# Performance work log

Hardware: AMD Instinct MI355X
Metric: run time of the kernel (lower is better)

Reference implementation:

```python
import jax, jax.numpy as jnp
import numpy as np

HID = 512; POOL = 4096; N_OBJ_CLS = 151; N_REL_CLS = 51; EMB = 200
N_OBJ = 1024; N_REL = 128

def conv(x, w, b, pad):
    y = jax.lax.conv_general_dilated(x, w, (1, 1), [(pad, pad), (pad, pad)],
                                     dimension_numbers=('NCHW', 'OIHW', 'NCHW'))
    return y + b[None, :, None, None]

def pool2(x):
    n, c, h, w = x.shape
    return x.reshape(n, c, h // 2, 2, w // 2, 2).mean(axis=(3, 5))

def setup_inputs() -> dict:
    ks = jax.random.split(jax.random.key(0), 40)
    s = 0.02
    d = {
        'obj_feats': jax.random.normal(ks[0], (N_OBJ, HID), jnp.float32),
        'obj_preds': jax.random.randint(ks[1], (N_OBJ,), 0, N_OBJ_CLS, jnp.int32),
        'pair_idx': jax.random.randint(ks[2], (N_REL, 2), 0, N_OBJ, jnp.int32),
        'union_features': jax.random.normal(ks[3], (N_REL, POOL), jnp.float32),
        'W_post_emb': jax.random.normal(ks[4], (HID, 2 * HID)) * s,
        'b_post_emb': jnp.zeros((2 * HID,)),
        'W_post_cat': jax.random.normal(ks[5], (2 * HID, POOL)) * s,
        'b_post_cat': jnp.zeros((POOL,)),
        'W_edge': jax.random.normal(ks[6], (POOL, HID)) * s,
        'b_edge': jnp.zeros((HID,)),
        'W_lin_rel': jax.random.normal(ks[7], (3 * HID, HID)) * s,
        'b_lin_rel': jnp.zeros((HID,)),
        'W_rel': jax.random.normal(ks[8], (HID, N_REL_CLS)) * s,
        'b_rel': jnp.zeros((N_REL_CLS,)),
        'freq_table': jax.random.normal(ks[9], (N_OBJ_CLS * N_OBJ_CLS, N_REL_CLS)) * s,
        'embed_vecs': jax.random.normal(ks[10], (N_OBJ + 1, EMB)) * 0.1,
        'cw1': jax.random.normal(ks[11], (64, 1, 5, 5)) * s, 'cb1': jnp.zeros((64,)),
        'cw2': jax.random.normal(ks[12], (128, 64, 3, 3)) * s, 'cb2': jnp.zeros((128,)),
        'cw3': jax.random.normal(ks[13], (256, 128, 3, 3)) * s, 'cb3': jnp.zeros((256,)),
        'cw4': jax.random.normal(ks[14], (512, 256, 3, 3)) * s, 'cb4': jnp.zeros((512,)),
        'cw5': jax.random.normal(ks[15], (384, 512, 1, 1)) * s, 'cb5': jnp.zeros((384,)),
        'cw6': jax.random.normal(ks[16], (4096, 384, 1, 1)) * s, 'cb6': jnp.zeros((4096,)),
        'Ww1': jax.random.normal(ks[17], (8192, 512)) * s, 'bw1': jnp.zeros((512,)),
        'Ww2': jax.random.normal(ks[18], (512, 4096)) * s, 'bw2': jnp.zeros((4096,)),
    }
    return d

def reference(obj_feats, obj_preds, pair_idx, union_features,
              W_post_emb, b_post_emb, W_post_cat, b_post_cat, W_edge, b_edge,
              W_lin_rel, b_lin_rel, W_rel, b_rel, freq_table, embed_vecs,
              cw1, cb1, cw2, cb2, cw3, cb3, cw4, cb4, cw5, cb5, cw6, cb6,
              Ww1, bw1, Ww2, bw2):
    p0 = pair_idx[:, 0]; p1 = pair_idx[:, 1]
    # post_emb -> head/tail reps, gather per pair (edge construction)
    edge_rep = obj_feats @ W_post_emb + b_post_emb          # [N_obj, 2H]
    head_rep = edge_rep[:, :HID]; tail_rep = edge_rep[:, HID:]
    prod_rep = jnp.concatenate([head_rep[p0], tail_rep[p1]], axis=-1)  # [R, 2H]
    # vision path with ctx gate
    ctx_gate = prod_rep @ W_post_cat + b_post_cat            # [R, POOL]
    visual_rep = ctx_gate * union_features
    # edge context (stand-in linear+relu projection to hidden)
    edge_feats = jax.nn.relu(visual_rep @ W_edge + b_edge)   # [R, H]
    # cat_pair fusion
    rel_sub = prod_rep[:, :HID]; rel_obj = prod_rep[:, HID:]
    rel_feats = jnp.concatenate([rel_sub, edge_feats, rel_obj], axis=-1) @ W_lin_rel + b_lin_rel
    rel_dists = rel_feats @ W_rel + b_rel                    # [R, 51]
    # frequency bias on predicted pair classes
    c0 = obj_preds[p0]; c1 = obj_preds[p1]
    rel_dists = rel_dists + freq_table[c0 * N_OBJ_CLS + c1]
    # word-image branch: outer product of pair word vectors -> conv tower (detached)
    oe = embed_vecs[p0 + 1]; se = embed_vecs[p1 + 1]         # [R, 200]
    x = (oe[:, :, None] * se[:, None, :])[:, None]           # [R, 1, 200, 200]
    x = pool2(jax.nn.relu(conv(x, cw1, cb1, 2)))             # [R, 64, 100, 100]
    x = pool2(jax.nn.relu(conv(x, cw2, cb2, 1)))             # [R, 128, 50, 50]
    x = pool2(jax.nn.relu(conv(x, cw3, cb3, 1)))             # [R, 256, 25, 25]
    x = jax.nn.relu(conv(x, cw4, cb4, 1))                    # [R, 512, 25, 25]
    x = x.mean(axis=(2, 3), keepdims=True)                   # adaptive avgpool -> [R,512,1,1]
    x = jax.nn.relu(conv(x, cw5, cb5, 0))
    x = conv(x, cw6, cb6, 0).reshape(-1, 4096)
    pwe = jax.lax.stop_gradient(x)                           # .detach() in original
    # word_feature MLP (eval: dropout off)
    h = jax.nn.relu(jnp.concatenate([pwe, union_features], axis=1) @ Ww1 + bw1)
    union_out = jax.nn.relu(h @ Ww2 + bw2)                   # [R, 4096]
    return rel_dists, union_out
```

## Files before the change

kernel.cpp:

```cpp
#include <hip/hip_runtime.h>
#include <hip/hip_bf16.h>


typedef __attribute__((ext_vector_type(8))) short  s16x8;
typedef __attribute__((ext_vector_type(4))) short  s16x4;
typedef __attribute__((ext_vector_type(4))) float  f32x4;

__device__ inline unsigned short f2bf(float f) {
    unsigned u = __builtin_bit_cast(unsigned, f);
    u = (u + 0x7FFF + ((u >> 16) & 1)) >> 16;
    return (unsigned short)u;
}
__device__ inline float bf2f(unsigned short s) {
    unsigned u = ((unsigned)s) << 16;
    return __builtin_bit_cast(float, u);
}

template<bool BT, bool RELU, bool MUL>
__global__ __launch_bounds__(256) void gemm_kernel(
    const float* __restrict__ A, const float* __restrict__ B,
    const float* __restrict__ bias, const float* __restrict__ mulp,
    float* __restrict__ C, int M, int N, int K)
{
    __shared__ float As[16][68];
    __shared__ float Bs[16][68];
    const int m0 = blockIdx.x * 64, n0 = blockIdx.y * 64;
    const int tid = threadIdx.x;
    const int ty = tid >> 4, tx = tid & 15;
    float acc[4][4] = {};
    for (int k0 = 0; k0 < K; k0 += 16) {
        {
            const int m = tid >> 2, kq = (tid & 3) << 2;
            const float4 a = *reinterpret_cast<const float4*>(A + (size_t)(m0 + m) * K + k0 + kq);
            As[kq + 0][m] = a.x; As[kq + 1][m] = a.y; As[kq + 2][m] = a.z; As[kq + 3][m] = a.w;
        }
        if (!BT) {
            const int kk = tid >> 4, nq = (tid & 15) << 2;
            const float4 b = *reinterpret_cast<const float4*>(B + (size_t)(k0 + kk) * N + n0 + nq);
            *reinterpret_cast<float4*>(&Bs[kk][nq]) = b;
        } else {
            const int nn = tid >> 2, kq = (tid & 3) << 2;
            const float4 b = *reinterpret_cast<const float4*>(B + (size_t)(n0 + nn) * K + k0 + kq);
            Bs[kq + 0][nn] = b.x; Bs[kq + 1][nn] = b.y; Bs[kq + 2][nn] = b.z; Bs[kq + 3][nn] = b.w;
        }
        __syncthreads();
#pragma unroll
        for (int k = 0; k < 16; ++k) {
            const float4 av = *reinterpret_cast<const float4*>(&As[k][ty << 2]);
            const float4 bv = *reinterpret_cast<const float4*>(&Bs[k][tx << 2]);
            acc[0][0] += av.x * bv.x; acc[0][1] += av.x * bv.y; acc[0][2] += av.x * bv.z; acc[0][3] += av.x * bv.w;
            acc[1][0] += av.y * bv.x; acc[1][1] += av.y * bv.y; acc[1][2] += av.y * bv.z; acc[1][3] += av.y * bv.w;
            acc[2][0] += av.z * bv.x; acc[2][1] += av.z * bv.y; acc[2][2] += av.z * bv.z; acc[2][3] += av.z * bv.w;
            acc[3][0] += av.w * bv.x; acc[3][1] += av.w * bv.y; acc[3][2] += av.w * bv.z; acc[3][3] += av.w * bv.w;
        }
        __syncthreads();
    }
#pragma unroll
    for (int i = 0; i < 4; ++i) {
        const int m = m0 + (ty << 2) + i;
#pragma unroll
        for (int j = 0; j < 4; ++j) {
            const int n = n0 + (tx << 2) + j;
            float v = acc[i][j] + bias[n];
            if (MUL) v *= mulp[(size_t)m * N + n];
            if (RELU) v = fmaxf(v, 0.f);
            C[(size_t)m * N + n] = v;
        }
    }
}

template<bool BT>
__global__ __launch_bounds__(256) void gemmsk_kernel(
    const float* __restrict__ A, const float* __restrict__ B,
    float* __restrict__ part, int M, int N, int K, int kchunk)
{
    __shared__ float As[16][68];
    __shared__ float Bs[16][68];
    const int m0 = blockIdx.x * 64, n0 = blockIdx.y * 64;
    const int kbeg = blockIdx.z * kchunk, kend = kbeg + kchunk;
    const int tid = threadIdx.x;
    const int ty = tid >> 4, tx = tid & 15;
    float acc[4][4] = {};
    for (int k0 = kbeg; k0 < kend; k0 += 16) {
        {
            const int m = tid >> 2, kq = (tid & 3) << 2;
            const float4 a = *reinterpret_cast<const float4*>(A + (size_t)(m0 + m) * K + k0 + kq);
            As[kq + 0][m] = a.x; As[kq + 1][m] = a.y; As[kq + 2][m] = a.z; As[kq + 3][m] = a.w;
        }
        if (!BT) {
            const int kk = tid >> 4, nq = (tid & 15) << 2;
            const float4 b = *reinterpret_cast<const float4*>(B + (size_t)(k0 + kk) * N + n0 + nq);
            *reinterpret_cast<float4*>(&Bs[kk][nq]) = b;
        } else {
            const int nn = tid >> 2, kq = (tid & 3) << 2;
            const float4 b = *reinterpret_cast<const float4*>(B + (size_t)(n0 + nn) * K + k0 + kq);
            Bs[kq + 0][nn] = b.x; Bs[kq + 1][nn] = b.y; Bs[kq + 2][nn] = b.z; Bs[kq + 3][nn] = b.w;
        }
        __syncthreads();
#pragma unroll
        for (int k = 0; k < 16; ++k) {
            const float4 av = *reinterpret_cast<const float4*>(&As[k][ty << 2]);
            const float4 bv = *reinterpret_cast<const float4*>(&Bs[k][tx << 2]);
            acc[0][0] += av.x * bv.x; acc[0][1] += av.x * bv.y; acc[0][2] += av.x * bv.z; acc[0][3] += av.x * bv.w;
            acc[1][0] += av.y * bv.x; acc[1][1] += av.y * bv.y; acc[1][2] += av.y * bv.z; acc[1][3] += av.y * bv.w;
            acc[2][0] += av.z * bv.x; acc[2][1] += av.z * bv.y; acc[2][2] += av.z * bv.z; acc[2][3] += av.z * bv.w;
            acc[3][0] += av.w * bv.x; acc[3][1] += av.w * bv.y; acc[3][2] += av.w * bv.z; acc[3][3] += av.w * bv.w;
        }
        __syncthreads();
    }
    float* pp = part + (size_t)blockIdx.z * M * N;
#pragma unroll
    for (int i = 0; i < 4; ++i) {
        const int m = m0 + (ty << 2) + i;
#pragma unroll
        for (int j = 0; j < 4; ++j)
            pp[(size_t)m * N + n0 + (tx << 2) + j] = acc[i][j];
    }
}

template<bool RELU, bool MUL>
__global__ __launch_bounds__(256) void reduce_kernel(
    const float* __restrict__ part, const float* __restrict__ bias,
    const float* __restrict__ mulp, float* __restrict__ C, int M, int N, int KS)
{
    const int idx = blockIdx.x * 256 + threadIdx.x;
    if (idx >= M * N) return;
    const int n = idx % N;
    float s = bias[n];
    for (int ks = 0; ks < KS; ++ks) s += part[(size_t)ks * M * N + idx];
    if (MUL) s *= mulp[idx];
    if (RELU) s = fmaxf(s, 0.f);
    C[idx] = s;
}

__global__ __launch_bounds__(256) void conv1_kernel(
    const float* __restrict__ emb, const int* __restrict__ pair,
    const float* __restrict__ wgt, const float* __restrict__ bias,
    unsigned short* __restrict__ out, int n0, long out_stride)
{
    __shared__ float soe[200], sse[200];
    __shared__ float r[8][5][204];
    const int n = blockIdx.x, gn = n0 + n;
    const int co0 = blockIdx.y * 8;
    const int tid = threadIdx.x;
    const float* oe = emb + (size_t)(pair[2 * gn + 0] + 1) * 200;
    const float* se = emb + (size_t)(pair[2 * gn + 1] + 1) * 200;
    if (tid < 200) { soe[tid] = oe[tid]; sse[tid] = se[tid]; }
    __syncthreads();
    for (int it = tid; it < 8000; it += 256) {
        const int c = it / 1000;
        const int rem = it - c * 1000;
        const int dy = rem / 200;
        const int j = rem - dy * 200;
        const float* w = wgt + (size_t)(co0 + c) * 25 + dy * 5;
        float s = 0.f;
#pragma unroll
        for (int dx = 0; dx < 5; ++dx) {
            const int jj = j + dx - 2;
            if ((unsigned)jj < 200u) s += w[dx] * sse[jj];
        }
        r[c][dy][j] = s;
    }
    __syncthreads();
    float bz[8];
#pragma unroll
    for (int c = 0; c < 8; ++c) bz[c] = bias[co0 + c];
    for (int p = tid; p < 10000; p += 256) {
        const int py = p / 100, px = p - py * 100;
        const int i0 = 2 * py - 2, j0 = 2 * px;
        float ov[6];
#pragma unroll
        for (int t = 0; t < 6; ++t) {
            const int ii = i0 + t;
            ov[t] = ((unsigned)ii < 200u) ? soe[ii] : 0.f;
        }
        unsigned short vals[8];
#pragma unroll
        for (int c = 0; c < 8; ++c) {
            float s00 = bz[c], s01 = bz[c], s10 = bz[c], s11 = bz[c];
#pragma unroll
            for (int dy = 0; dy < 5; ++dy) {
                const float2 rv = *reinterpret_cast<const float2*>(&r[c][dy][j0]);
                s00 += ov[dy]     * rv.x; s01 += ov[dy]     * rv.y;
                s10 += ov[dy + 1] * rv.x; s11 += ov[dy + 1] * rv.y;
            }
            vals[c] = f2bf(0.25f * (fmaxf(s00, 0.f) + fmaxf(s01, 0.f) +
                                    fmaxf(s10, 0.f) + fmaxf(s11, 0.f)));
        }
        *reinterpret_cast<s16x8*>(out + (size_t)n * out_stride + (size_t)p * 64 + co0) =
            *reinterpret_cast<s16x8*>(vals);
    }
}

__global__ __launch_bounds__(256) void frepack_kernel(
    const float* __restrict__ w, unsigned short* __restrict__ o,
    int CO, int CI, int NSTEP, int CLOG)
{
    const int id = blockIdx.x * 256 + threadIdx.x;
    const int total = (CO >> 4) * NSTEP * 64;
    if (id >= total) return;
    const int lane = id & 63;
    const int gt = id >> 6;
    const int t = gt % NSTEP, g = gt / NSTEP;
    const int co = g * 16 + (lane & 15);
    unsigned short r[8];
#pragma unroll
    for (int e = 0; e < 8; ++e) {
        const int kk = t * 32 + ((lane >> 4) << 3) + e;
        const int ci = kk & (CI - 1);
        const int dydx = kk >> CLOG;
        const int dy = dydx / 3, dx = dydx - dy * 3;
        r[e] = f2bf(w[((size_t)(co * CI + ci) * 3 + dy) * 3 + dx]);
    }
    *reinterpret_cast<s16x8*>(o + (size_t)id * 8) = *reinterpret_cast<s16x8*>(r);
}

template<int CI, int W, int CO_BLK, int PX_BLK, int WM, int WN, int MF, int NF>
__global__ __launch_bounds__(256) void convlds_kernel(
    const unsigned short* __restrict__ in, const unsigned short* __restrict__ wf,
    const float* __restrict__ bias, unsigned short* __restrict__ out,
    int CO, long in_stride, long out_stride)
{
    constexpr int NPIX = W * W;
    constexpr int K = 9 * CI;
    constexpr int NSTEP = K / 32;
    constexpr int NC = CI / 8;
    constexpr int NCL = (NC == 8) ? 3 : (NC == 16) ? 4 : 5;
    constexpr int CLOG = (CI == 64) ? 6 : (CI == 128) ? 7 : 8;
    constexpr int STAGE_PX = PX_BLK + 2 * W + 2;
    constexpr int TOT16 = STAGE_PX * NC;
    constexpr int WCO = CO_BLK / WM;
    constexpr int WPX = PX_BLK / WN;
    __shared__ unsigned short lds[STAGE_PX * CI + 8];

    const int tid = threadIdx.x;
    const unsigned short* inp = in + (size_t)blockIdx.z * in_stride;
    const int p_base = blockIdx.x * PX_BLK;
    const int q0 = p_base - (W + 1);

    for (int i = tid; i < TOT16; i += 256) {
        const int s = i >> NCL;
        const int c = i & (NC - 1);
        int q = q0 + s;
        q = q < 0 ? 0 : (q >= NPIX ? NPIX - 1 : q);
        s16x8 v = *reinterpret_cast<const s16x8*>(inp + (size_t)q * CI + c * 8);
        const int perm = c ^ (s & (NC - 1));
        *reinterpret_cast<s16x8*>(&lds[(s * NC + perm) * 8]) = v;
    }
    if (tid == 0) *reinterpret_cast<s16x8*>(&lds[STAGE_PX * CI]) = s16x8{};
    __syncthreads();

    const int lane = tid & 63, wid = tid >> 6;
    const int wm = wid % WM, wn = wid / WM;
    const int lhi = lane >> 4, llo = lane & 15;
    const int g0 = (blockIdx.y * CO_BLK + wm * WCO) >> 4;

    const unsigned short* pa[MF];
#pragma unroll
    for (int mf = 0; mf < MF; ++mf)
        pa[mf] = wf + ((size_t)(g0 + mf) * NSTEP * 64 + lane) * 8;

    int sb[NF], py[NF], px[NF];
    bool vp[NF];
#pragma unroll
    for (int nf = 0; nf < NF; ++nf) {
        const int p = p_base + wn * WPX + nf * 16 + llo;
        vp[nf] = p < NPIX;
        py[nf] = p / W; px[nf] = p - py[nf] * W;
        sb[nf] = p - q0;
    }

    f32x4 acc[MF][NF] = {};
#pragma unroll 2
    for (int t = 0; t < NSTEP; ++t) {
        const int k0 = t * 32;
        const int dydx = k0 >> CLOG;
        const int dy = dydx / 3, dx = dydx - dy * 3;
        const int delta = (dy - 1) * W + (dx - 1);
        const int cb = ((k0 & (CI - 1)) >> 3) + lhi;
        s16x8 a[MF], b[NF];
#pragma unroll
        for (int mf = 0; mf < MF; ++mf)
            a[mf] = *reinterpret_cast<const s16x8*>(pa[mf] + (size_t)t * 512);
#pragma unroll
        for (int nf = 0; nf < NF; ++nf) {
            const int s = sb[nf] + delta;
            const int iy = py[nf] + dy - 1, ix = px[nf] + dx - 1;
            const bool ok = vp[nf] && (unsigned)iy < (unsigned)W && (unsigned)ix < (unsigned)W;
            const int ofs = ok ? (s * NC + (cb ^ (s & (NC - 1)))) : TOT16;
            b[nf] = *reinterpret_cast<const s16x8*>(&lds[ofs * 8]);
        }
#pragma unroll
        for (int mf = 0; mf < MF; ++mf)
#pragma unroll
            for (int nf = 0; nf < NF; ++nf)
                acc[mf][nf] = __builtin_amdgcn_mfma_f32_16x16x32_bf16(a[mf], b[nf], acc[mf][nf], 0, 0, 0);
    }

    unsigned short* outp = out + (size_t)blockIdx.z * out_stride;
#pragma unroll
    for (int mf = 0; mf < MF; ++mf) {
        const int co = blockIdx.y * CO_BLK + wm * WCO + mf * 16 + lhi * 4;
        const float b0 = bias[co], b1 = bias[co + 1], b2 = bias[co + 2], b3 = bias[co + 3];
#pragma unroll
        for (int nf = 0; nf < NF; ++nf) {
            if (!vp[nf]) continue;
            const int p = p_base + wn * WPX + nf * 16 + llo;
            f32x4 a = acc[mf][nf];
            unsigned short r[4];
            r[0] = f2bf(fmaxf(a.x + b0, 0.f));
            r[1] = f2bf(fmaxf(a.y + b1, 0.f));
            r[2] = f2bf(fmaxf(a.z + b2, 0.f));
            r[3] = f2bf(fmaxf(a.w + b3, 0.f));
            *reinterpret_cast<s16x4*>(outp + (size_t)p * CO + co) = *reinterpret_cast<s16x4*>(r);
        }
    }
}

template<int OHW, int CO>
__global__ __launch_bounds__(256) void pool_kernel(
    const unsigned short* __restrict__ in, unsigned short* __restrict__ out,
    long in_stride, long out_stride)
{
    constexpr int W2 = OHW * 2;
    constexpr int C8 = CO / 8;
    constexpr int ITEMS = OHW * C8;
    const int n = blockIdx.x, y = blockIdx.y;
    const unsigned short* ip = in + (size_t)n * in_stride + (size_t)(2 * y) * W2 * CO;
    unsigned short* op = out + (size_t)n * out_stride + (size_t)y * OHW * CO;
    for (int it = threadIdx.x; it < ITEMS; it += 256) {
        const int x = it >> ((C8 == 16) ? 4 : 5);
        const int c0 = (it - x * C8) * 8;
        const unsigned short* q = ip + (size_t)(2 * x) * CO + c0;
        s16x8 a = *reinterpret_cast<const s16x8*>(q);
        s16x8 b = *reinterpret_cast<const s16x8*>(q + CO);
        s16x8 c = *reinterpret_cast<const s16x8*>(q + (size_t)W2 * CO);
        s16x8 d = *reinterpret_cast<const s16x8*>(q + (size_t)W2 * CO + CO);
        s16x8 r;
#pragma unroll
        for (int j = 0; j < 8; ++j)
            r[j] = (short)f2bf(0.25f * (bf2f((unsigned short)a[j]) + bf2f((unsigned short)b[j]) +
                                        bf2f((unsigned short)c[j]) + bf2f((unsigned short)d[j])));
        *reinterpret_cast<s16x8*>(op + (size_t)x * CO + c0) = r;
    }
}

__global__ __launch_bounds__(256) void gap_kernel(
    const unsigned short* __restrict__ in, float* __restrict__ gap,
    int n0, long in_stride)
{
    __shared__ float sm[4][512];
    const unsigned short* ip = in + (size_t)blockIdx.x * in_stride;
    const int g = threadIdx.x >> 6;
    const int c8 = threadIdx.x & 63;
    float s[8] = {};
    for (int p = g; p < 625; p += 4) {
        s16x8 v = *reinterpret_cast<const s16x8*>(ip + (size_t)p * 512 + c8 * 8);
#pragma unroll
        for (int j = 0; j < 8; ++j) s[j] += bf2f((unsigned short)v[j]);
    }
#pragma unroll
    for (int j = 0; j < 8; ++j) sm[g][c8 * 8 + j] = s[j];
    __syncthreads();
    if (g == 0) {
#pragma unroll
        for (int j = 0; j < 8; ++j) {
            const int ch = c8 * 8 + j;
            const float t = sm[0][ch] + sm[1][ch] + sm[2][ch] + sm[3][ch];
            gap[(size_t)(n0 + blockIdx.x) * 512 + ch] = t * (1.f / 625.f);
        }
    }
}

__global__ __launch_bounds__(256) void prod_kernel(
    const float* __restrict__ er, const int* __restrict__ pair, float* __restrict__ pr)
{
    const int r = blockIdx.x;
    const int p0 = pair[2 * r], p1 = pair[2 * r + 1];
    for (int i = threadIdx.x; i < 1024; i += 256) {
        const int src = (i < 512) ? p0 : p1;
        pr[(size_t)r * 1024 + i] = er[(size_t)src * 1024 + i];
    }
}

__global__ __launch_bounds__(256) void rcat_kernel(
    const float* __restrict__ prodr, const float* __restrict__ ef, float* __restrict__ rc)
{
    const int r = blockIdx.x;
    for (int i = threadIdx.x; i < 1536; i += 256) {
        float v;
        if (i < 512)       v = prodr[(size_t)r * 1024 + i];
        else if (i < 1024) v = ef[(size_t)r * 512 + (i - 512)];
        else               v = prodr[(size_t)r * 1024 + (i - 1024) + 512];
        rc[(size_t)r * 1536 + i] = v;
    }
}

__global__ __launch_bounds__(256) void cat8_kernel(
    const float* __restrict__ pwe, const float* __restrict__ un, float* __restrict__ cat)
{
    const int r = blockIdx.x;
    for (int i = threadIdx.x; i < 8192; i += 256) {
        cat[(size_t)r * 8192 + i] = (i < 4096) ? pwe[(size_t)r * 4096 + i]
                                               : un[(size_t)r * 4096 + (i - 4096)];
    }
}

__global__ __launch_bounds__(256) void reldist_kernel(
    const float* __restrict__ rf, const float* __restrict__ Wr, const float* __restrict__ br,
    const float* __restrict__ freq, const int* __restrict__ preds,
    const int* __restrict__ pair, float* __restrict__ out)
{
    const int idx = blockIdx.x * 256 + threadIdx.x;
    if (idx >= 128 * 51) return;
    const int r = idx / 51, j = idx - r * 51;
    const float* a = rf + (size_t)r * 512;
    float s = br[j];
    for (int k = 0; k < 512; ++k) s += a[k] * Wr[(size_t)k * 51 + j];
    const int c0 = preds[pair[2 * r]], c1 = preds[pair[2 * r + 1]];
    s += freq[((size_t)c0 * 151 + c1) * 51 + j];
    out[idx] = s;
}

extern "C" void kernel_launch(void* const* d_in, const int* in_sizes, int n_in,
                              void* d_out, int out_size, void* d_ws, size_t ws_size,
                              hipStream_t stream)
{
    const float* obj_feats  = (const float*)d_in[0];
    const int*   obj_preds  = (const int*)  d_in[1];
    const int*   pair       = (const int*)  d_in[2];
    const float* unionf     = (const float*)d_in[3];
    const float* W_post_emb = (const float*)d_in[4];
    const float* b_post_emb = (const float*)d_in[5];
    const float* W_post_cat = (const float*)d_in[6];
    const float* b_post_cat = (const float*)d_in[7];
    const float* W_edge     = (const float*)d_in[8];
    const float* b_edge     = (const float*)d_in[9];
    const float* W_lin      = (const float*)d_in[10];
    const float* b_lin      = (const float*)d_in[11];
    const float* W_rel      = (const float*)d_in[12];
    const float* b_rel      = (const float*)d_in[13];
    const float* freq       = (const float*)d_in[14];
    const float* emb        = (const float*)d_in[15];
    const float* cw1 = (const float*)d_in[16]; const float* cb1 = (const float*)d_in[17];
    const float* cw2 = (const float*)d_in[18]; const float* cb2 = (const float*)d_in[19];
    const float* cw3 = (const float*)d_in[20]; const float* cb3 = (const float*)d_in[21];
    const float* cw4 = (const float*)d_in[22]; const float* cb4 = (const float*)d_in[23];
    const float* cw5 = (const float*)d_in[24]; const float* cb5 = (const float*)d_in[25];
    const float* cw6 = (const float*)d_in[26]; const float* cb6 = (const float*)d_in[27];
    const float* Ww1 = (const float*)d_in[28]; const float* bw1 = (const float*)d_in[29];
    const float* Ww2 = (const float*)d_in[30]; const float* bw2 = (const float*)d_in[31];
    float* out = (float*)d_out;

    float* ws = (float*)d_ws;
    float* edge_rep   = ws;
    float* prodr      = edge_rep + 1048576;
    float* visual     = prodr + 131072;
    float* edge_feats = visual + 524288;
    float* rcat       = edge_feats + 65536;
    float* rel_feats  = rcat + 196608;
    float* gap        = rel_feats + 65536;
    float* x5         = gap + 65536;
    float* pwe        = x5 + 49152;
    float* cat8       = pwe + 524288;
    float* hbuf       = cat8 + 1048576;
    float* part       = hbuf + 65536;
    const size_t persist_f32 = 3784704ull + 2097152ull;

    unsigned short* wsu = (unsigned short*)(ws + persist_f32);
    unsigned short* w2r = wsu;
    unsigned short* w3r = w2r + 73728;
    unsigned short* w4r = w3r + 294912;
    unsigned short* actA = w4r + 1179648;

    int C = 128;
    const size_t base_bytes = persist_f32 * 4 + 1548288ull * 2;
    while (C > 1 && base_bytes + (size_t)C * 1920000ull * 2 > ws_size) C >>= 1;
    unsigned short* actB = actA + (size_t)C * 640000;

    gemm_kernel<false,false,false><<<dim3(16,16),256,0,stream>>>(obj_feats, W_post_emb, b_post_emb, nullptr, edge_rep, 1024,1024,512);
    prod_kernel<<<dim3(128),256,0,stream>>>(edge_rep, pair, prodr);
    gemmsk_kernel<false><<<dim3(2,64,4),256,0,stream>>>(prodr, W_post_cat, part, 128,4096,1024, 256);
    reduce_kernel<false,true ><<<dim3(2048),256,0,stream>>>(part, b_post_cat, unionf, visual, 128,4096,4);
    gemmsk_kernel<false><<<dim3(2,8,16),256,0,stream>>>(visual, W_edge, part, 128,512,4096, 256);
    reduce_kernel<true ,false><<<dim3(256),256,0,stream>>>(part, b_edge, nullptr, edge_feats, 128,512,16);
    rcat_kernel<<<dim3(128),256,0,stream>>>(prodr, edge_feats, rcat);
    gemmsk_kernel<false><<<dim3(2,8,8),256,0,stream>>>(rcat, W_lin, part, 128,512,1536, 192);
    reduce_kernel<false,false><<<dim3(256),256,0,stream>>>(part, b_lin, nullptr, rel_feats, 128,512,8);
    reldist_kernel<<<dim3(26),256,0,stream>>>(rel_feats, W_rel, b_rel, freq, obj_preds, pair, out);

    frepack_kernel<<<dim3(36), 256,0,stream>>>(cw2, w2r, 128, 64, 18, 6);
    frepack_kernel<<<dim3(144),256,0,stream>>>(cw3, w3r, 256, 128, 36, 7);
    frepack_kernel<<<dim3(576),256,0,stream>>>(cw4, w4r, 512, 256, 72, 8);

    for (int n0 = 0; n0 < 128; n0 += C) {
        conv1_kernel<<<dim3(C,8),256,0,stream>>>(emb, pair, cw1, cb1, actA, n0, 640000);
        convlds_kernel<64,100,128,128,2,2,4,4><<<dim3(79,1,C),256,0,stream>>>(actA, w2r, cb2, actB, 128, 640000, 1280000);
        pool_kernel<50,128><<<dim3(C,50),256,0,stream>>>(actB, actA, 1280000, 640000);
        convlds_kernel<128,50,256,64,4,1,4,4><<<dim3(40,1,C),256,0,stream>>>(actA, w3r, cb3, actB, 256, 640000, 1280000);
        pool_kernel<25,256><<<dim3(C,25),256,0,stream>>>(actB, actA, 1280000, 640000);
        convlds_kernel<256,25,512,32,4,1,8,2><<<dim3(20,1,C),256,0,stream>>>(actA, w4r, cb4, actB, 512, 640000, 1280000);
        gap_kernel<<<dim3(C),256,0,stream>>>(actB, gap, n0, 1280000);
    }

    gemmsk_kernel<true ><<<dim3(2,6,8),256,0,stream>>>(gap, cw5, part, 128,384,512, 64);
    reduce_kernel<true ,false><<<dim3(192),256,0,stream>>>(part, cb5, nullptr, x5, 128,384,8);
    gemmsk_kernel<true ><<<dim3(2,64,4),256,0,stream>>>(x5, cw6, part, 128,4096,384, 96);
    reduce_kernel<false,false><<<dim3(2048),256,0,stream>>>(part, cb6, nullptr, pwe, 128,4096,4);

    cat8_kernel<<<dim3(128),256,0,stream>>>(pwe, unionf, cat8);
    gemmsk_kernel<false><<<dim3(2,8,32),256,0,stream>>>(cat8, Ww1, part, 128,512,8192, 256);
    reduce_kernel<true ,false><<<dim3(256),256,0,stream>>>(part, bw1, nullptr, hbuf, 128,512,32);
    gemmsk_kernel<false><<<dim3(2,64,4),256,0,stream>>>(hbuf, Ww2, part, 128,4096,512, 128);
    reduce_kernel<true ,false><<<dim3(2048),256,0,stream>>>(part, bw2, nullptr, out + 6528, 128,4096,4);
}
```

Measured before the change: 1.564 ms.

## Fuse pooling into conv staging, gather pairs in GEMM, drop concat copies

Removes the standalone 2x2 average-pool kernels by letting the next conv's LDS staging load four input pixels and average them on the fly. Also fuses the pair gather into the post_cat GEMM A-load, splits the concat GEMM into two launches writing adjacent split-K partials, and merges the three weight-repack launches into one. The aim is fewer launches and less intermediate global traffic. In exchange, each pooled pixel is recomputed for the halo rows that neighbouring conv blocks stage, and the conv staging loop gets heavier.

```diff
diff --git a/kernel.cpp b/kernel.cpp
--- a/kernel.cpp
+++ b/kernel.cpp
@@ -95,6 +95,52 @@
             const int nn = tid >> 2, kq = (tid & 3) << 2;
             const float4 b = *reinterpret_cast<const float4*>(B + (size_t)(n0 + nn) * K + k0 + kq);
             Bs[kq + 0][nn] = b.x; Bs[kq + 1][nn] = b.y; Bs[kq + 2][nn] = b.z; Bs[kq + 3][nn] = b.w;
+        }
+        __syncthreads();
+#pragma unroll
+        for (int k = 0; k < 16; ++k) {
+            const float4 av = *reinterpret_cast<const float4*>(&As[k][ty << 2]);
+            const float4 bv = *reinterpret_cast<const float4*>(&Bs[k][tx << 2]);
+            acc[0][0] += av.x * bv.x; acc[0][1] += av.x * bv.y; acc[0][2] += av.x * bv.z; acc[0][3] += av.x * bv.w;
+            acc[1][0] += av.y * bv.x; acc[1][1] += av.y * bv.y; acc[1][2] += av.y * bv.z; acc[1][3] += av.y * bv.w;
+            acc[2][0] += av.z * bv.x; acc[2][1] += av.z * bv.y; acc[2][2] += av.z * bv.z; acc[2][3] += av.z * bv.w;
+            acc[3][0] += av.w * bv.x; acc[3][1] += av.w * bv.y; acc[3][2] += av.w * bv.z; acc[3][3] += av.w * bv.w;
+        }
+        __syncthreads();
+    }
+    float* pp = part + (size_t)blockIdx.z * M * N;
+#pragma unroll
+    for (int i = 0; i < 4; ++i) {
+        const int m = m0 + (ty << 2) + i;
+#pragma unroll
+        for (int j = 0; j < 4; ++j)
+            pp[(size_t)m * N + n0 + (tx << 2) + j] = acc[i][j];
+    }
+}
+
+__global__ __launch_bounds__(256) void gemmsk_gather_kernel(
+    const float* __restrict__ er, const int* __restrict__ pair,
+    const float* __restrict__ B, float* __restrict__ part, int M, int N, int kchunk)
+{
+    __shared__ float As[16][68];
+    __shared__ float Bs[16][68];
+    const int m0 = blockIdx.x * 64, n0 = blockIdx.y * 64;
+    const int kbeg = blockIdx.z * kchunk, kend = kbeg + kchunk;
+    const int sel = (kbeg >= 512) ? 1 : 0;
+    const int tid = threadIdx.x;
+    const int ty = tid >> 4, tx = tid & 15;
+    float acc[4][4] = {};
+    for (int k0 = kbeg; k0 < kend; k0 += 16) {
+        {
+            const int m = tid >> 2, kq = (tid & 3) << 2;
+            const int src = pair[2 * (m0 + m) + sel];
+            const float4 a = *reinterpret_cast<const float4*>(er + (size_t)src * 1024 + k0 + kq);
+            As[kq + 0][m] = a.x; As[kq + 1][m] = a.y; As[kq + 2][m] = a.z; As[kq + 3][m] = a.w;
+        }
+        {
+            const int kk = tid >> 4, nq = (tid & 15) << 2;
+            const float4 b = *reinterpret_cast<const float4*>(B + (size_t)(k0 + kk) * N + n0 + nq);
+            *reinterpret_cast<float4*>(&Bs[kk][nq]) = b;
         }
         __syncthreads();
 #pragma unroll
@@ -192,13 +238,16 @@
     }
 }
 
-__global__ __launch_bounds__(256) void frepack_kernel(
-    const float* __restrict__ w, unsigned short* __restrict__ o,
-    int CO, int CI, int NSTEP, int CLOG)
-{
-    const int id = blockIdx.x * 256 + threadIdx.x;
-    const int total = (CO >> 4) * NSTEP * 64;
-    if (id >= total) return;
+__global__ __launch_bounds__(256) void frepack3_kernel(
+    const float* __restrict__ w2, const float* __restrict__ w3, const float* __restrict__ w4,
+    unsigned short* __restrict__ o2, unsigned short* __restrict__ o3, unsigned short* __restrict__ o4)
+{
+    const int b = blockIdx.x;
+    const float* w; unsigned short* o; int CI, NSTEP, CLOG, base;
+    if (b < 36)       { w = w2; o = o2; CI = 64;  NSTEP = 18; CLOG = 6; base = 0; }
+    else if (b < 180) { w = w3; o = o3; CI = 128; NSTEP = 36; CLOG = 7; base = 36; }
+    else              { w = w4; o = o4; CI = 256; NSTEP = 72; CLOG = 8; base = 180; }
+    const int id = (b - base) * 256 + threadIdx.x;
     const int lane = id & 63;
     const int gt = id >> 6;
     const int t = gt % NSTEP, g = gt / NSTEP;
@@ -215,7 +264,7 @@
     *reinterpret_cast<s16x8*>(o + (size_t)id * 8) = *reinterpret_cast<s16x8*>(r);
 }
 
-template<int CI, int W, int CO_BLK, int PX_BLK, int WM, int WN, int MF, int NF>
+template<int CI, int W, int CO_BLK, int PX_BLK, int WM, int WN, int MF, int NF, bool PIN>
 __global__ __launch_bounds__(256) void convlds_kernel(
     const unsigned short* __restrict__ in, const unsigned short* __restrict__ wf,
     const float* __restrict__ bias, unsigned short* __restrict__ out,
@@ -231,7 +280,7 @@
     constexpr int TOT16 = STAGE_PX * NC;
     constexpr int WCO = CO_BLK / WM;
     constexpr int WPX = PX_BLK / WN;
-    __shared__ unsigned short lds[STAGE_PX * CI + 8];
+    __shared__ unsigned short lds[(TOT16 + NC) * 8];
 
     const int tid = threadIdx.x;
     const unsigned short* inp = in + (size_t)blockIdx.z * in_stride;
@@ -243,11 +292,26 @@
         const int c = i & (NC - 1);
         int q = q0 + s;
         q = q < 0 ? 0 : (q >= NPIX ? NPIX - 1 : q);
-        s16x8 v = *reinterpret_cast<const s16x8*>(inp + (size_t)q * CI + c * 8);
+        s16x8 v;
+        if (PIN) {
+            constexpr int WR = 2 * W;
+            const int qy = q / W, qx = q - qy * W;
+            const unsigned short* src = inp + ((size_t)(2 * qy) * WR + 2 * qx) * CI + c * 8;
+            s16x8 va = *reinterpret_cast<const s16x8*>(src);
+            s16x8 vb = *reinterpret_cast<const s16x8*>(src + CI);
+            s16x8 vc = *reinterpret_cast<const s16x8*>(src + (size_t)WR * CI);
+            s16x8 vd = *reinterpret_cast<const s16x8*>(src + (size_t)WR * CI + CI);
+#pragma unroll
+            for (int j = 0; j < 8; ++j)
+                v[j] = (short)f2bf(0.25f * (bf2f((unsigned short)va[j]) + bf2f((unsigned short)vb[j]) +
+                                            bf2f((unsigned short)vc[j]) + bf2f((unsigned short)vd[j])));
+        } else {
+            v = *reinterpret_cast<const s16x8*>(inp + (size_t)q * CI + c * 8);
+        }
         const int perm = c ^ (s & (NC - 1));
         *reinterpret_cast<s16x8*>(&lds[(s * NC + perm) * 8]) = v;
     }
-    if (tid == 0) *reinterpret_cast<s16x8*>(&lds[STAGE_PX * CI]) = s16x8{};
+    if (tid < NC) *reinterpret_cast<s16x8*>(&lds[(TOT16 + tid) * 8]) = s16x8{};
     __syncthreads();
 
     const int lane = tid & 63, wid = tid >> 6;
@@ -317,34 +381,6 @@
     }
 }
 
-template<int OHW, int CO>
-__global__ __launch_bounds__(256) void pool_kernel(
-    const unsigned short* __restrict__ in, unsigned short* __restrict__ out,
-    long in_stride, long out_stride)
-{
-    constexpr int W2 = OHW * 2;
-    constexpr int C8 = CO / 8;
-    constexpr int ITEMS = OHW * C8;
-    const int n = blockIdx.x, y = blockIdx.y;
-    const unsigned short* ip = in + (size_t)n * in_stride + (size_t)(2 * y) * W2 * CO;
-    unsigned short* op = out + (size_t)n * out_stride + (size_t)y * OHW * CO;
-    for (int it = threadIdx.x; it < ITEMS; it += 256) {
-        const int x = it >> ((C8 == 16) ? 4 : 5);
-        const int c0 = (it - x * C8) * 8;
-        const unsigned short* q = ip + (size_t)(2 * x) * CO + c0;
-        s16x8 a = *reinterpret_cast<const s16x8*>(q);
-        s16x8 b = *reinterpret_cast<const s16x8*>(q + CO);
-        s16x8 c = *reinterpret_cast<const s16x8*>(q + (size_t)W2 * CO);
-        s16x8 d = *reinterpret_cast<const s16x8*>(q + (size_t)W2 * CO + CO);
-        s16x8 r;
-#pragma unroll
-        for (int j = 0; j < 8; ++j)
-            r[j] = (short)f2bf(0.25f * (bf2f((unsigned short)a[j]) + bf2f((unsigned short)b[j]) +
-                                        bf2f((unsigned short)c[j]) + bf2f((unsigned short)d[j])));
-        *reinterpret_cast<s16x8*>(op + (size_t)x * CO + c0) = r;
-    }
-}
-
 __global__ __launch_bounds__(256) void gap_kernel(
     const unsigned short* __restrict__ in, float* __restrict__ gap,
     int n0, long in_stride)
@@ -372,37 +408,18 @@
     }
 }
 
-__global__ __launch_bounds__(256) void prod_kernel(
-    const float* __restrict__ er, const int* __restrict__ pair, float* __restrict__ pr)
+__global__ __launch_bounds__(256) void rcat_kernel(
+    const float* __restrict__ er, const int* __restrict__ pair,
+    const float* __restrict__ ef, float* __restrict__ rc)
 {
     const int r = blockIdx.x;
     const int p0 = pair[2 * r], p1 = pair[2 * r + 1];
-    for (int i = threadIdx.x; i < 1024; i += 256) {
-        const int src = (i < 512) ? p0 : p1;
-        pr[(size_t)r * 1024 + i] = er[(size_t)src * 1024 + i];
-    }
-}
-
-__global__ __launch_bounds__(256) void rcat_kernel(
-    const float* __restrict__ prodr, const float* __restrict__ ef, float* __restrict__ rc)
-{
-    const int r = blockIdx.x;
     for (int i = threadIdx.x; i < 1536; i += 256) {
         float v;
-        if (i < 512)       v = prodr[(size_t)r * 1024 + i];
+        if (i < 512)       v = er[(size_t)p0 * 1024 + i];
         else if (i < 1024) v = ef[(size_t)r * 512 + (i - 512)];
-        else               v = prodr[(size_t)r * 1024 + (i - 1024) + 512];
+        else               v = er[(size_t)p1 * 1024 + (i - 512)];
         rc[(size_t)r * 1536 + i] = v;
-    }
-}
-
-__global__ __launch_bounds__(256) void cat8_kernel(
-    const float* __restrict__ pwe, const float* __restrict__ un, float* __restrict__ cat)
-{
-    const int r = blockIdx.x;
-    for (int i = threadIdx.x; i < 8192; i += 256) {
-        cat[(size_t)r * 8192 + i] = (i < 4096) ? pwe[(size_t)r * 4096 + i]
-                                               : un[(size_t)r * 4096 + (i - 4096)];
     }
 }
 
@@ -454,18 +471,16 @@
 
     float* ws = (float*)d_ws;
     float* edge_rep   = ws;
-    float* prodr      = edge_rep + 1048576;
-    float* visual     = prodr + 131072;
+    float* visual     = edge_rep + 1048576;
     float* edge_feats = visual + 524288;
     float* rcat       = edge_feats + 65536;
     float* rel_feats  = rcat + 196608;
     float* gap        = rel_feats + 65536;
     float* x5         = gap + 65536;
     float* pwe        = x5 + 49152;
-    float* cat8       = pwe + 524288;
-    float* hbuf       = cat8 + 1048576;
+    float* hbuf       = pwe + 524288;
     float* part       = hbuf + 65536;
-    const size_t persist_f32 = 3784704ull + 2097152ull;
+    const size_t persist_f32 = 2555904ull + 2097152ull;
 
     unsigned short* wsu = (unsigned short*)(ws + persist_f32);
     unsigned short* w2r = wsu;
@@ -479,27 +494,22 @@
     unsigned short* actB = actA + (size_t)C * 640000;
 
     gemm_kernel<false,false,false><<<dim3(16,16),256,0,stream>>>(obj_feats, W_post_emb, b_post_emb, nullptr, edge_rep, 1024,1024,512);
-    prod_kernel<<<dim3(128),256,0,stream>>>(edge_rep, pair, prodr);
-    gemmsk_kernel<false><<<dim3(2,64,4),256,0,stream>>>(prodr, W_post_cat, part, 128,4096,1024, 256);
+    gemmsk_gather_kernel<<<dim3(2,64,4),256,0,stream>>>(edge_rep, pair, W_post_cat, part, 128,4096, 256);
     reduce_kernel<false,true ><<<dim3(2048),256,0,stream>>>(part, b_post_cat, unionf, visual, 128,4096,4);
     gemmsk_kernel<false><<<dim3(2,8,16),256,0,stream>>>(visual, W_edge, part, 128,512,4096, 256);
     reduce_kernel<true ,false><<<dim3(256),256,0,stream>>>(part, b_edge, nullptr, edge_feats, 128,512,16);
-    rcat_kernel<<<dim3(128),256,0,stream>>>(prodr, edge_feats, rcat);
+    rcat_kernel<<<dim3(128),256,0,stream>>>(edge_rep, pair, edge_feats, rcat);
     gemmsk_kernel<false><<<dim3(2,8,8),256,0,stream>>>(rcat, W_lin, part, 128,512,1536, 192);
     reduce_kernel<false,false><<<dim3(256),256,0,stream>>>(part, b_lin, nullptr, rel_feats, 128,512,8);
     reldist_kernel<<<dim3(26),256,0,stream>>>(rel_feats, W_rel, b_rel, freq, obj_preds, pair, out);
 
-    frepack_kernel<<<dim3(36), 256,0,stream>>>(cw2, w2r, 128, 64, 18, 6);
-    frepack_kernel<<<dim3(144),256,0,stream>>>(cw3, w3r, 256, 128, 36, 7);
-    frepack_kernel<<<dim3(576),256,0,stream>>>(cw4, w4r, 512, 256, 72, 8);
+    frepack3_kernel<<<dim3(756),256,0,stream>>>(cw2, cw3, cw4, w2r, w3r, w4r);
 
     for (int n0 = 0; n0 < 128; n0 += C) {
         conv1_kernel<<<dim3(C,8),256,0,stream>>>(emb, pair, cw1, cb1, actA, n0, 640000);
-        convlds_kernel<64,100,128,128,2,2,4,4><<<dim3(79,1,C),256,0,stream>>>(actA, w2r, cb2, actB, 128, 640000, 1280000);
-        pool_kernel<50,128><<<dim3(C,50),256,0,stream>>>(actB, actA, 1280000, 640000);
-        convlds_kernel<128,50,256,64,4,1,4,4><<<dim3(40,1,C),256,0,stream>>>(actA, w3r, cb3, actB, 256, 640000, 1280000);
-        pool_kernel<25,256><<<dim3(C,25),256,0,stream>>>(actB, actA, 1280000, 640000);
-        convlds_kernel<256,25,512,32,4,1,8,2><<<dim3(20,1,C),256,0,stream>>>(actA, w4r, cb4, actB, 512, 640000, 1280000);
+        convlds_kernel<64,100,128,128,2,2,4,4,false><<<dim3(79,1,C),256,0,stream>>>(actA, w2r, cb2, actB, 128, 640000, 1280000);
+        convlds_kernel<128,50,256,64,4,1,4,4,true ><<<dim3(40,1,C),256,0,stream>>>(actB, w3r, cb3, actA, 256, 1280000, 640000);
+        convlds_kernel<256,25,512,32,4,1,8,2,true ><<<dim3(20,1,C),256,0,stream>>>(actA, w4r, cb4, actB, 512, 640000, 1280000);
         gap_kernel<<<dim3(C),256,0,stream>>>(actB, gap, n0, 1280000);
     }
 
@@ -508,8 +518,8 @@
     gemmsk_kernel<true ><<<dim3(2,64,4),256,0,stream>>>(x5, cw6, part, 128,4096,384, 96);
     reduce_kernel<false,false><<<dim3(2048),256,0,stream>>>(part, cb6, nullptr, pwe, 128,4096,4);
 
-    cat8_kernel<<<dim3(128),256,0,stream>>>(pwe, unionf, cat8);
-    gemmsk_kernel<false><<<dim3(2,8,32),256,0,stream>>>(cat8, Ww1, part, 128,512,8192, 256);
+    gemmsk_kernel<false><<<dim3(2,8,16),256,0,stream>>>(pwe, Ww1, part, 128,512,4096, 256);
+    gemmsk_kernel<false><<<dim3(2,8,16),256,0,stream>>>(unionf, Ww1 + (size_t)4096 * 512, part + (size_t)16 * 65536, 128,512,4096, 256);
     reduce_kernel<true ,false><<<dim3(256),256,0,stream>>>(part, bw1, nullptr, hbuf, 128,512,32);
     gemmsk_kernel<false><<<dim3(2,64,4),256,0,stream>>>(hbuf, Ww2, part, 128,4096,512, 128);
     reduce_kernel<true ,false><<<dim3(2048),256,0,stream>>>(part, bw2, nullptr, out + 6528, 128,4096,4);
```

New measurement: 1.326 ms. 15.2% less time.
